# Optimization experiments

Hardware: AMD Instinct MI355X
Metric: run time of the kernel (lower is better)

Reference implementation:

```python
import jax, jax.numpy as jnp
import numpy as np

D_MODEL = 1024
N_HEADS = 16
HEAD_DIM = D_MODEL // N_HEADS
ROPE_DIM = HEAD_DIM  # rope_fraction=1.0
BASE = 10000.0


def _rope_cos_sin(T, dtype):
    theta = 1.0 / (BASE ** (jnp.arange(0, ROPE_DIM, 2, dtype=jnp.float32) / ROPE_DIM))
    t = jnp.arange(T, dtype=jnp.float32)
    freqs = jnp.outer(t, theta)                     # [T, ROPE_DIM/2]
    emb = jnp.concatenate([freqs, freqs], axis=-1)  # [T, ROPE_DIM]
    return jnp.cos(emb).astype(dtype), jnp.sin(emb).astype(dtype)


def _rotate(x, cos, sin):
    # x: [B, H, T, D]; apply rotary to first ROPE_DIM dims (here full D)
    x_rope, x_pass = x[..., :ROPE_DIM], x[..., ROPE_DIM:]
    x1, x2 = x_rope[..., :ROPE_DIM // 2], x_rope[..., ROPE_DIM // 2:]
    rotated = jnp.concatenate([-x2, x1], axis=-1)
    x_rope = x_rope * cos + rotated * sin
    return jnp.concatenate([x_rope, x_pass], axis=-1)


def setup_inputs() -> dict:
    key = jax.random.key(0)
    k1, k2, k3 = jax.random.split(key, 3)
    x = jax.random.normal(k1, (4, 2048, D_MODEL), dtype=jnp.float32)
    w_qkv = jax.random.normal(k2, (3 * D_MODEL, D_MODEL), dtype=jnp.float32) * (1.0 / np.sqrt(D_MODEL))
    w_out = jax.random.normal(k3, (D_MODEL, D_MODEL), dtype=jnp.float32) * (1.0 / np.sqrt(D_MODEL))
    return {"x": x, "w_qkv": w_qkv, "w_out": w_out}


def reference(x, w_qkv, w_out):
    B, T, C = x.shape
    qkv = jnp.einsum('btc,oc->bto', x, w_qkv)  # Linear: x @ W.T
    q, k, v = jnp.split(qkv, 3, axis=-1)

    def reshape(t):
        return t.reshape(B, T, N_HEADS, HEAD_DIM).transpose(0, 2, 1, 3)  # [B,H,T,D]

    q, k, v = reshape(q), reshape(k), reshape(v)

    cos, sin = _rope_cos_sin(T, x.dtype)  # [T, ROPE_DIM]
    cos = cos[None, None, :, :]
    sin = sin[None, None, :, :]
    q = _rotate(q, cos, sin)
    k = _rotate(k, cos, sin)

    scale = 1.0 / np.sqrt(HEAD_DIM).astype(np.float32)
    attn = jnp.einsum('bhqd,bhkd->bhqk', q, k) * scale
    causal = jnp.tril(jnp.ones((T, T), dtype=bool))
    attn = jnp.where(causal[None, None], attn, jnp.finfo(attn.dtype).min)
    attn = jax.nn.softmax(attn, axis=-1)
    out = jnp.einsum('bhqk,bhkd->bhqd', attn, v)
    out = out.transpose(0, 2, 1, 3).reshape(B, T, C)
    return jnp.einsum('btc,oc->bto', out, w_out)
```

## Files before the change

kernel.cpp:

```cpp
#include <hip/hip_runtime.h>

typedef unsigned short u16;
typedef __attribute__((ext_vector_type(8))) short v8s;
typedef __attribute__((ext_vector_type(4))) float v4f;

__device__ __forceinline__ u16 f2bf(float f) {
  unsigned u = __float_as_uint(f);
  u += 0x7FFF + ((u >> 16) & 1);
  return (u16)(u >> 16);
}

__device__ __forceinline__ unsigned pk2bf(float lo, float hi) {
  unsigned a = __float_as_uint(lo) + 0x8000u;
  unsigned b = __float_as_uint(hi) + 0x8000u;
  return __builtin_amdgcn_perm(b, a, 0x07060302);
}

__device__ __forceinline__ v4f zero4() {
  v4f z; z[0] = 0.f; z[1] = 0.f; z[2] = 0.f; z[3] = 0.f; return z;
}

__device__ __forceinline__ void async16(const u16* g, u16* l) {
  __builtin_amdgcn_global_load_lds(
      (const __attribute__((address_space(1))) unsigned int*)g,
      (__attribute__((address_space(3))) unsigned int*)l, 16, 0, 0);
}

__device__ __forceinline__ void fast_sincos(float x, float* s, float* c) {
  float k = rintf(x * 0.15915494309189535f);
  float r = __builtin_fmaf(k, -6.28125f, x);
  r = __builtin_fmaf(k, -0.0019353071795864769f, r);
  *s = __sinf(r);
  *c = __cosf(r);
}

#define ATTN_SCL (0.125f * 1.4426950408889634f)

__global__ __launch_bounds__(256) void cast_all_k(const float* __restrict__ x,
                                                  const float* __restrict__ wq,
                                                  const float* __restrict__ wo,
                                                  u16* __restrict__ dst) {
  int i = blockIdx.x * 256 + threadIdx.x;
  const float4* s;
  int si;
  if (i < 2097152) { s = (const float4*)x;  si = i; }
  else if (i < 2883584) { s = (const float4*)wq; si = i - 2097152; }
  else { s = (const float4*)wo; si = i - 2883584; }
  float4 v = s[si];
  ((ushort4*)dst)[i] = make_ushort4(f2bf(v.x), f2bf(v.y), f2bf(v.z), f2bf(v.w));
}


__device__ __forceinline__ void gemm_core(const u16* __restrict__ A,
                                          const u16* __restrict__ B, int K,
                                          int row0, int col0, u16* As, u16* Bs,
                                          v4f acc[4][4]) {
  const int tid = threadIdx.x;
  const int lane = tid & 63;
  const int wm = (tid >> 7) & 1;
  const int wn = (tid >> 6) & 1;
  const int ln = lane & 15, quad = lane >> 4;
#pragma unroll
  for (int i = 0; i < 4; ++i)
#pragma unroll
    for (int j = 0; j < 4; ++j) acc[i][j] = zero4();
  const int rA = tid >> 3;
  const int cA = (((tid & 7) ^ (rA & 7)) << 3);
  for (int kt = 0; kt < K; kt += 64) {
#pragma unroll
    for (int i = 0; i < 4; ++i) {
      async16(A + (size_t)(row0 + i * 32 + rA) * K + kt + cA, As + i * 2048 + tid * 8);
      async16(B + (size_t)(col0 + i * 32 + rA) * K + kt + cA, Bs + i * 2048 + tid * 8);
    }
    __syncthreads();
#pragma unroll
    for (int kk = 0; kk < 2; ++kk) {
      const int go = (((kk * 4 + quad) ^ (ln & 7)) << 3);
      v8s af[4], bfr[4];
#pragma unroll
      for (int i = 0; i < 4; ++i) {
        af[i]  = *(const v8s*)(As + (wm * 64 + i * 16 + ln) * 64 + go);
        bfr[i] = *(const v8s*)(Bs + (wn * 64 + i * 16 + ln) * 64 + go);
      }
      __builtin_amdgcn_s_setprio(1);
#pragma unroll
      for (int i = 0; i < 4; ++i)
#pragma unroll
        for (int j = 0; j < 4; ++j)
          acc[i][j] = __builtin_amdgcn_mfma_f32_16x16x32_bf16(af[i], bfr[j], acc[i][j], 0, 0, 0);
      __builtin_amdgcn_s_setprio(0);
    }
    __syncthreads();
  }
}

__global__ __launch_bounds__(256) void gemm_qkv_rope(const u16* __restrict__ A,
                                                     const u16* __restrict__ B,
                                                     u16* __restrict__ Qh,
                                                     u16* __restrict__ Kh,
                                                     u16* __restrict__ Vt) {
  __shared__ __align__(16) u16 As[8192];
  __shared__ __align__(16) u16 Bs[8192];
  v4f acc[4][4];
  const int row0 = blockIdx.x * 128, col0 = blockIdx.y * 128;
  gemm_core(A, B, 1024, row0, col0, As, Bs, acc);
  const int tid = threadIdx.x, lane = tid & 63;
  const int wm = (tid >> 7) & 1, wn = (tid >> 6) & 1;
  const int ln = lane & 15, quad = lane >> 4;
  const int colbase = col0 + wn * 64;
  const int seg = colbase >> 10;
  const int h = (colbase & 1023) >> 6;
  if (seg < 2) {
    u16* dst = (seg == 0) ? Qh : Kh;
    const float oscl = (seg == 0) ? ATTN_SCL : 1.0f;
#pragma unroll
    for (int i = 0; i < 4; ++i) {
#pragma unroll
      for (int r = 0; r < 4; ++r) {
        int row = row0 + wm * 64 + i * 16 + quad * 4 + r;
        int b = row >> 11, t = row & 2047;
        size_t base = ((size_t)(b * 16 + h) * 2048 + t) * 64;
#pragma unroll
        for (int j = 0; j < 2; ++j) {
          int d1 = j * 16 + ln;
          float theta = exp2f((float)d1 * -0.4152410118609203f);
          float sn, cs;
          fast_sincos((float)t * theta, &sn, &cs);
          float v1 = acc[i][j][r], v2 = acc[i][j + 2][r];
          dst[base + d1]      = f2bf((v1 * cs - v2 * sn) * oscl);
          dst[base + d1 + 32] = f2bf((v2 * cs + v1 * sn) * oscl);
        }
      }
    }
  } else {
#pragma unroll
    for (int i = 0; i < 4; ++i)
#pragma unroll
      for (int j = 0; j < 4; ++j) {
        int d = j * 16 + ln;
#pragma unroll
        for (int r = 0; r < 4; ++r) {
          int row = row0 + wm * 64 + i * 16 + quad * 4 + r;
          int b = row >> 11, t = row & 2047;
          Vt[((size_t)(b * 16 + h) * 64 + d) * 2048 + t] = f2bf(acc[i][j][r]);
        }
      }
  }
}

__global__ __launch_bounds__(256) void gemm_out_k(const u16* __restrict__ A,
                                                  const u16* __restrict__ B,
                                                  float* __restrict__ C) {
  __shared__ __align__(16) u16 As[8192];
  __shared__ __align__(16) u16 Bs[8192];
  v4f acc[4][4];
  const int row0 = blockIdx.x * 128, col0 = blockIdx.y * 128;
  gemm_core(A, B, 1024, row0, col0, As, Bs, acc);
  const int tid = threadIdx.x, lane = tid & 63;
  const int wm = (tid >> 7) & 1, wn = (tid >> 6) & 1;
  const int ln = lane & 15, quad = lane >> 4;
#pragma unroll
  for (int i = 0; i < 4; ++i)
#pragma unroll
    for (int r = 0; r < 4; ++r) {
      int row = row0 + wm * 64 + i * 16 + quad * 4 + r;
#pragma unroll
      for (int j = 0; j < 4; ++j) {
        int col = col0 + wn * 64 + j * 16 + ln;
        C[(size_t)row * 1024 + col] = acc[i][j][r];
      }
    }
}


template <bool MASKED>
__device__ __forceinline__ void qk_sm_pv(const v8s ak[2][4], const v8s av[2][4],
                                         u16* Pw, const v8s aq[2], v4f od[4],
                                         float& l, int s0, int qrow, int ln,
                                         int quad, int swz) {
  v4f sc[4];
#pragma unroll
  for (int kf = 0; kf < 4; ++kf) sc[kf] = zero4();
#pragma unroll
  for (int kk = 0; kk < 2; ++kk) {
    __builtin_amdgcn_s_setprio(1);
#pragma unroll
    for (int kf = 0; kf < 4; ++kf)
      sc[kf] = __builtin_amdgcn_mfma_f32_16x16x32_bf16(ak[kk][kf], aq[kk], sc[kf], 0, 0, 0);
    __builtin_amdgcn_s_setprio(0);
  }
  float ls = 0.f;
#pragma unroll
  for (int kf = 0; kf < 4; ++kf) {
    float p[4];
#pragma unroll
    for (int r = 0; r < 4; ++r) {
      float v = sc[kf][r];
      if (MASKED) {
        int key = s0 + kf * 16 + quad * 4 + r;
        v = (key <= qrow) ? v : -3.0e38f;
      }
      p[r] = exp2f(v);
    }
    ls += (p[0] + p[1]) + (p[2] + p[3]);
    uint2 pk;
    pk.x = pk2bf(p[0], p[1]);
    pk.y = pk2bf(p[2], p[3]);
    *(uint2*)(Pw + ln * 64 + (((kf * 4 + quad) ^ swz) << 2)) = pk;
  }
  l += ls;
#pragma unroll
  for (int kk = 0; kk < 2; ++kk) {
    v8s bp = *(const v8s*)(Pw + ln * 64 + (((kk * 8 + quad * 2) ^ swz) << 2));
    __builtin_amdgcn_s_setprio(1);
#pragma unroll
    for (int df = 0; df < 4; ++df)
      od[df] = __builtin_amdgcn_mfma_f32_16x16x32_bf16(av[kk][df], bp, od[df], 0, 0, 0);
    __builtin_amdgcn_s_setprio(0);
  }
}

__device__ __forceinline__ void flash_epi(float l, const v4f od[4], int t,
                                          int b, int h, int quad,
                                          u16* __restrict__ O) {
  float lt = l;
  lt += __shfl_xor(lt, 16);
  lt += __shfl_xor(lt, 32);
  float inv = 1.0f / lt;
  size_t obase = ((size_t)b * 2048 + t) * 1024 + h * 64;
#pragma unroll
  for (int df = 0; df < 4; ++df) {
    ushort4 o;
    o.x = f2bf(od[df][0] * inv);
    o.y = f2bf(od[df][1] * inv);
    o.z = f2bf(od[df][2] * inv);
    o.w = f2bf(od[df][3] * inv);
    *(ushort4*)(O + obase + df * 16 + quad * 4) = o;
  }
}

__global__ __launch_bounds__(256, 2) void flash_k(const u16* __restrict__ Q,
                                                  const u16* __restrict__ Kh,
                                                  const u16* __restrict__ V,
                                                  u16* __restrict__ O) {
  __shared__ __align__(16) u16 Ks[2][4096];
  __shared__ __align__(16) u16 Vs[2][4096];
  __shared__ __align__(16) u16 Ps[4096];
  const int tid = threadIdx.x;
  const int lane = tid & 63, w = tid >> 6;
  const int ln = lane & 15, quad = lane >> 4;
  const int swz = (lane & 7) << 1;
  const int qx = 15 - blockIdx.y;
  const int bh = blockIdx.x;
  const int b = bh >> 4, h = bh & 15;
  const size_t qoff = (size_t)bh * 2048 * 64;
  u16* Pw = Ps + w * 1024;

  const int rS = tid >> 3;
  const int cS = (((tid & 7) ^ (rS & 7)) << 3);
  const u16* Kbase = Kh + qoff;
  const u16* Vbase = V + (size_t)bh * 131072;

  const int nt = 2 * qx + 2;
  const int diag = 2 * qx + (w >> 1);
  const int S0 = qx * 128 + w * 32;
  const int qrow0 = S0 + ln, qrow1 = S0 + 16 + ln;
  v8s aq0[2], aq1[2];
#pragma unroll
  for (int kk = 0; kk < 2; ++kk) {
    aq0[kk] = *(const v8s*)(Q + qoff + (size_t)(S0 + ln) * 64 + kk * 32 + quad * 8);
    aq1[kk] = *(const v8s*)(Q + qoff + (size_t)(S0 + 16 + ln) * 64 + kk * 32 + quad * 8);
  }
  float l0 = 0.f, l1 = 0.f;
  v4f od0[4], od1[4];
#pragma unroll
  for (int df = 0; df < 4; ++df) { od0[df] = zero4(); od1[df] = zero4(); }

  {
    async16(Kbase + (size_t)rS * 64 + cS, Ks[0] + tid * 8);
    async16(Kbase + (size_t)(32 + rS) * 64 + cS, Ks[0] + 2048 + tid * 8);
    async16(Vbase + (size_t)rS * 2048 + cS, Vs[0] + tid * 8);
    async16(Vbase + (size_t)(rS + 32) * 2048 + cS, Vs[0] + 2048 + tid * 8);
  }
  for (int it = 0; it < nt; ++it) {
    __syncthreads();
    if (it + 1 < nt) {
      const int s1 = (it + 1) * 64;
      u16* kd = Ks[(it + 1) & 1];
      u16* vd = Vs[(it + 1) & 1];
      async16(Kbase + (size_t)(s1 + rS) * 64 + cS, kd + tid * 8);
      async16(Kbase + (size_t)(s1 + 32 + rS) * 64 + cS, kd + 2048 + tid * 8);
      async16(Vbase + (size_t)rS * 2048 + s1 + cS, vd + tid * 8);
      async16(Vbase + (size_t)(rS + 32) * 2048 + s1 + cS, vd + 2048 + tid * 8);
    }
    if (it <= diag) {
      const u16* Kc = Ks[it & 1];
      const u16* Vc = Vs[it & 1];
      v8s ak[2][4], av[2][4];
#pragma unroll
      for (int kk = 0; kk < 2; ++kk) {
        const int go = (((kk * 4 + quad) ^ (ln & 7)) << 3);
#pragma unroll
        for (int i = 0; i < 4; ++i) {
          ak[kk][i] = *(const v8s*)(Kc + (i * 16 + ln) * 64 + go);
          av[kk][i] = *(const v8s*)(Vc + (i * 16 + ln) * 64 + go);
        }
      }
      const int s0 = it * 64;
      if (it == diag) {
        qk_sm_pv<true>(ak, av, Pw, aq0, od0, l0, s0, qrow0, ln, quad, swz);
        qk_sm_pv<true>(ak, av, Pw, aq1, od1, l1, s0, qrow1, ln, quad, swz);
      } else {
        qk_sm_pv<false>(ak, av, Pw, aq0, od0, l0, s0, qrow0, ln, quad, swz);
        qk_sm_pv<false>(ak, av, Pw, aq1, od1, l1, s0, qrow1, ln, quad, swz);
      }
    }
  }

  flash_epi(l0, od0, S0 + ln, b, h, quad, O);
  flash_epi(l1, od1, S0 + 16 + ln, b, h, quad, O);
}

extern "C" void kernel_launch(void* const* d_in, const int* in_sizes, int n_in,
                              void* d_out, int out_size, void* d_ws, size_t ws_size,
                              hipStream_t stream) {
  const float* x     = (const float*)d_in[0];
  const float* w_qkv = (const float*)d_in[1];
  const float* w_out = (const float*)d_in[2];
  float* out = (float*)d_out;
  char* ws = (char*)d_ws;
  u16* xb    = (u16*)(ws);
  u16* wqkvb = (u16*)(ws + 16777216);
  u16* woutb = (u16*)(ws + 23068672);
  u16* qh    = (u16*)(ws + 25165824);
  u16* kh    = (u16*)(ws + 41943040);
  u16* vt    = (u16*)(ws + 58720256);
  u16* oa    = (u16*)(ws + 75497472);

  cast_all_k<<<12288, 256, 0, stream>>>(x, w_qkv, w_out, (u16*)ws);
  gemm_qkv_rope<<<dim3(64, 24), 256, 0, stream>>>(xb, wqkvb, qh, kh, vt);
  flash_k<<<dim3(64, 16), 256, 0, stream>>>(qh, kh, vt, oa);
  gemm_out_k<<<dim3(64, 8), 256, 0, stream>>>(oa, woutb, out);
}
```

Measured before the change: 246.5 us.

## Rewrite QKV GEMM with 256x256 tiles, 8 waves, and double-buffered async staging

The QKV projection GEMM moves from 128x128 tiles on 4 waves to 256x256 tiles on 8 waves. It uses 128KB of dynamic LDS with double-buffered, XOR-swizzled async global-to-LDS loads, and interleaves fragment reads, MFMA groups and barriers in a ping-pong schedule. The goal is more operand reuse per LDS byte and hiding global load latency behind MFMA work. In exchange the block count drops to 384, which may underfill the CUs, and the kernel needs more registers and a larger LDS footprint.

```diff
diff --git a/kernel.cpp b/kernel.cpp
--- a/kernel.cpp
+++ b/kernel.cpp
@@ -94,19 +94,169 @@
   }
 }
 
-__global__ __launch_bounds__(256) void gemm_qkv_rope(const u16* __restrict__ A,
-                                                     const u16* __restrict__ B,
-                                                     u16* __restrict__ Qh,
-                                                     u16* __restrict__ Kh,
-                                                     u16* __restrict__ Vt) {
-  __shared__ __align__(16) u16 As[8192];
-  __shared__ __align__(16) u16 Bs[8192];
-  v4f acc[4][4];
-  const int row0 = blockIdx.x * 128, col0 = blockIdx.y * 128;
-  gemm_core(A, B, 1024, row0, col0, As, Bs, acc);
-  const int tid = threadIdx.x, lane = tid & 63;
-  const int wm = (tid >> 7) & 1, wn = (tid >> 6) & 1;
+__global__ __launch_bounds__(512, 2) void gemm_qkv_rope(const u16* __restrict__ A,
+                                                        const u16* __restrict__ B,
+                                                        u16* __restrict__ Qh,
+                                                        u16* __restrict__ Kh,
+                                                        u16* __restrict__ Vt) {
+  extern __shared__ __align__(16) u16 lds8[];
+  u16* As = lds8;
+  u16* Bs = lds8 + 32768;
+  const int tid = threadIdx.x;
+  const int lane = tid & 63, w = tid >> 6;
+  const int wm = w >> 2, wn = w & 3;
   const int ln = lane & 15, quad = lane >> 4;
+  const int row0 = blockIdx.x * 256, col0 = blockIdx.y * 256;
+  const int NT = 16;
+
+  v4f acc[8][4];
+#pragma unroll
+  for (int m = 0; m < 8; ++m)
+#pragma unroll
+    for (int n = 0; n < 4; ++n) acc[m][n] = zero4();
+
+  auto stage = [&](const u16* src, int rowbase, int kcol, u16* dst) {
+#pragma unroll
+    for (int qq = 0; qq < 2; ++qq) {
+      int g = tid + qq * 512;
+      int r = g >> 3, slot = g & 7;
+      int sc = (slot ^ (r & 7)) << 3;
+      async16(src + (size_t)(rowbase + r) * 1024 + kcol + sc, dst + g * 8);
+    }
+  };
+
+  stage(A, row0,       0,  As);
+  stage(A, row0 + 128, 0,  As + 8192);
+  stage(B, col0,       0,  Bs);
+  stage(B, col0 + 128, 0,  Bs + 8192);
+  stage(A, row0,       64, As + 16384);
+  stage(A, row0 + 128, 64, As + 24576);
+  asm volatile("s_waitcnt vmcnt(4)" ::: "memory");
+  __builtin_amdgcn_sched_barrier(0);
+  __builtin_amdgcn_s_barrier();
+  __builtin_amdgcn_sched_barrier(0);
+
+  const int bhf = wn >> 1;
+  const int brow0 = (wn & 1) * 64;
+
+#pragma unroll 2
+  for (int k = 0; k < NT; ++k) {
+    const int bk = k & 1;
+    const u16* Ab = As + bk * 16384 + wm * 8192;
+    const u16* Bb = Bs + bk * 16384 + bhf * 8192 + brow0 * 64;
+    v8s afA[2][4], bfLo[2][2], bfHi[2][2];
+
+#pragma unroll
+    for (int kk = 0; kk < 2; ++kk) {
+      const int go = (((kk * 4 + quad) ^ (ln & 7)) << 3);
+#pragma unroll
+      for (int m = 0; m < 4; ++m)
+        afA[kk][m] = *(const v8s*)(Ab + (m * 16 + ln) * 64 + go);
+#pragma unroll
+      for (int n = 0; n < 2; ++n)
+        bfLo[kk][n] = *(const v8s*)(Bb + (n * 16 + ln) * 64 + go);
+    }
+    if (k + 1 < NT) {
+      u16* bd = Bs + (bk ^ 1) * 16384;
+      stage(B, col0,       (k + 1) * 64, bd);
+      stage(B, col0 + 128, (k + 1) * 64, bd + 8192);
+    }
+    __builtin_amdgcn_sched_barrier(0);
+    __builtin_amdgcn_s_barrier();
+    __builtin_amdgcn_sched_barrier(0);
+    __builtin_amdgcn_s_setprio(1);
+#pragma unroll
+    for (int kk = 0; kk < 2; ++kk)
+#pragma unroll
+      for (int m = 0; m < 4; ++m)
+#pragma unroll
+        for (int n = 0; n < 2; ++n)
+          acc[m][n] = __builtin_amdgcn_mfma_f32_16x16x32_bf16(afA[kk][m], bfLo[kk][n], acc[m][n], 0, 0, 0);
+    __builtin_amdgcn_s_setprio(0);
+    __builtin_amdgcn_sched_barrier(0);
+    __builtin_amdgcn_s_barrier();
+    __builtin_amdgcn_sched_barrier(0);
+
+#pragma unroll
+    for (int kk = 0; kk < 2; ++kk) {
+      const int go = (((kk * 4 + quad) ^ (ln & 7)) << 3);
+#pragma unroll
+      for (int n = 0; n < 2; ++n)
+        bfHi[kk][n] = *(const v8s*)(Bb + ((n + 2) * 16 + ln) * 64 + go);
+    }
+    __builtin_amdgcn_sched_barrier(0);
+    __builtin_amdgcn_s_barrier();
+    __builtin_amdgcn_sched_barrier(0);
+    __builtin_amdgcn_s_setprio(1);
+#pragma unroll
+    for (int kk = 0; kk < 2; ++kk)
+#pragma unroll
+      for (int m = 0; m < 4; ++m)
+#pragma unroll
+        for (int n = 0; n < 2; ++n)
+          acc[m][n + 2] = __builtin_amdgcn_mfma_f32_16x16x32_bf16(afA[kk][m], bfHi[kk][n], acc[m][n + 2], 0, 0, 0);
+    __builtin_amdgcn_s_setprio(0);
+    __builtin_amdgcn_sched_barrier(0);
+    __builtin_amdgcn_s_barrier();
+    __builtin_amdgcn_sched_barrier(0);
+
+#pragma unroll
+    for (int kk = 0; kk < 2; ++kk) {
+      const int go = (((kk * 4 + quad) ^ (ln & 7)) << 3);
+#pragma unroll
+      for (int m = 0; m < 4; ++m)
+        afA[kk][m] = *(const v8s*)(Ab + (64 + m * 16 + ln) * 64 + go);
+    }
+    __builtin_amdgcn_sched_barrier(0);
+    __builtin_amdgcn_s_barrier();
+    __builtin_amdgcn_sched_barrier(0);
+    __builtin_amdgcn_s_setprio(1);
+#pragma unroll
+    for (int kk = 0; kk < 2; ++kk)
+#pragma unroll
+      for (int m = 0; m < 4; ++m)
+#pragma unroll
+        for (int n = 0; n < 2; ++n)
+          acc[m + 4][n + 2] = __builtin_amdgcn_mfma_f32_16x16x32_bf16(afA[kk][m], bfHi[kk][n], acc[m + 4][n + 2], 0, 0, 0);
+    __builtin_amdgcn_s_setprio(0);
+    __builtin_amdgcn_sched_barrier(0);
+    __builtin_amdgcn_s_barrier();
+    __builtin_amdgcn_sched_barrier(0);
+
+#pragma unroll
+    for (int kk = 0; kk < 2; ++kk) {
+      const int go = (((kk * 4 + quad) ^ (ln & 7)) << 3);
+#pragma unroll
+      for (int n = 0; n < 2; ++n)
+        bfLo[kk][n] = *(const v8s*)(Bb + (n * 16 + ln) * 64 + go);
+    }
+    if (k + 2 < NT) {
+      u16* ad = As + bk * 16384;
+      stage(A, row0,       (k + 2) * 64, ad);
+      stage(A, row0 + 128, (k + 2) * 64, ad + 8192);
+    }
+    __builtin_amdgcn_sched_barrier(0);
+    __builtin_amdgcn_s_barrier();
+    __builtin_amdgcn_sched_barrier(0);
+    __builtin_amdgcn_s_setprio(1);
+#pragma unroll
+    for (int kk = 0; kk < 2; ++kk)
+#pragma unroll
+      for (int m = 0; m < 4; ++m)
+#pragma unroll
+        for (int n = 0; n < 2; ++n)
+          acc[m + 4][n] = __builtin_amdgcn_mfma_f32_16x16x32_bf16(afA[kk][m], bfLo[kk][n], acc[m + 4][n], 0, 0, 0);
+    __builtin_amdgcn_s_setprio(0);
+    if (k == NT - 2) {
+      asm volatile("s_waitcnt vmcnt(0)" ::: "memory");
+    } else {
+      asm volatile("s_waitcnt vmcnt(4)" ::: "memory");
+    }
+    __builtin_amdgcn_sched_barrier(0);
+    __builtin_amdgcn_s_barrier();
+    __builtin_amdgcn_sched_barrier(0);
+  }
+
   const int colbase = col0 + wn * 64;
   const int seg = colbase >> 10;
   const int h = (colbase & 1023) >> 6;
@@ -114,10 +264,10 @@
     u16* dst = (seg == 0) ? Qh : Kh;
     const float oscl = (seg == 0) ? ATTN_SCL : 1.0f;
 #pragma unroll
-    for (int i = 0; i < 4; ++i) {
+    for (int mf = 0; mf < 8; ++mf) {
 #pragma unroll
       for (int r = 0; r < 4; ++r) {
-        int row = row0 + wm * 64 + i * 16 + quad * 4 + r;
+        int row = row0 + wm * 128 + mf * 16 + quad * 4 + r;
         int b = row >> 11, t = row & 2047;
         size_t base = ((size_t)(b * 16 + h) * 2048 + t) * 64;
 #pragma unroll
@@ -126,7 +276,7 @@
           float theta = exp2f((float)d1 * -0.4152410118609203f);
           float sn, cs;
           fast_sincos((float)t * theta, &sn, &cs);
-          float v1 = acc[i][j][r], v2 = acc[i][j + 2][r];
+          float v1 = acc[mf][j][r], v2 = acc[mf][j + 2][r];
           dst[base + d1]      = f2bf((v1 * cs - v2 * sn) * oscl);
           dst[base + d1 + 32] = f2bf((v2 * cs + v1 * sn) * oscl);
         }
@@ -134,15 +284,15 @@
     }
   } else {
 #pragma unroll
-    for (int i = 0; i < 4; ++i)
-#pragma unroll
-      for (int j = 0; j < 4; ++j) {
-        int d = j * 16 + ln;
+    for (int mf = 0; mf < 8; ++mf)
+#pragma unroll
+      for (int nf = 0; nf < 4; ++nf) {
+        int d = nf * 16 + ln;
 #pragma unroll
         for (int r = 0; r < 4; ++r) {
-          int row = row0 + wm * 64 + i * 16 + quad * 4 + r;
+          int row = row0 + wm * 128 + mf * 16 + quad * 4 + r;
           int b = row >> 11, t = row & 2047;
-          Vt[((size_t)(b * 16 + h) * 64 + d) * 2048 + t] = f2bf(acc[i][j][r]);
+          Vt[((size_t)(b * 16 + h) * 64 + d) * 2048 + t] = f2bf(acc[mf][nf][r]);
         }
       }
   }
@@ -171,7 +321,6 @@
       }
     }
 }
-
 
 template <bool MASKED>
 __device__ __forceinline__ void qk_sm_pv(const v8s ak[2][4], const v8s av[2][4],
@@ -337,8 +486,15 @@
   u16* vt    = (u16*)(ws + 58720256);
   u16* oa    = (u16*)(ws + 75497472);
 
+  static bool attr_set = false;
+  if (!attr_set) {
+    hipFuncSetAttribute(reinterpret_cast<const void*>(gemm_qkv_rope),
+                        hipFuncAttributeMaxDynamicSharedMemorySize, 131072);
+    attr_set = true;
+  }
+
   cast_all_k<<<12288, 256, 0, stream>>>(x, w_qkv, w_out, (u16*)ws);
-  gemm_qkv_rope<<<dim3(64, 24), 256, 0, stream>>>(xb, wqkvb, qh, kh, vt);
+  gemm_qkv_rope<<<dim3(32, 12), 512, 131072, stream>>>(xb, wqkvb, qh, kh, vt);
   flash_k<<<dim3(64, 16), 256, 0, stream>>>(qh, kh, vt, oa);
   gemm_out_k<<<dim3(64, 8), 256, 0, stream>>>(oa, woutb, out);
 }
```

After: 249.9 us. No clear change (+1.4%).
